# Kernel optimization log

Measured on AMD Instinct MI355X. Metric: run time of the kernel, lower is better.

## Reference

```python
import jax, jax.numpy as jnp
import numpy as np

ITERS = 10   # self.iters
REG = 0.1    # self.reg
EPS = 1e-12  # F.normalize eps


def setup_inputs() -> dict:
    key = jax.random.key(0)
    k1, k2 = jax.random.split(key)
    b, n_s, h = 64, 512, 1024
    x = jax.random.normal(k1, (b, n_s, h), dtype=jnp.float32)
    y = jax.random.normal(k2, (b, n_s, h), dtype=jnp.float32)
    return {"x": x, "y": y}


def _l2_normalize(t):
    n = jnp.sqrt(jnp.sum(t * t, axis=-1, keepdims=True))
    return t / jnp.maximum(n, EPS)


def reference(x, y):
    # CosineScorer.score(x, y, get_diag=False) with temperature=1
    xn = _l2_normalize(x)
    yn = _l2_normalize(y)
    scores = jnp.einsum('bmh,bnh->bmn', xn, yn)  # (b, n_s, n_s)
    b, m, n = scores.shape

    # uniform log marginals: -log(n_s)
    log_mu = jnp.full((b, m), -jnp.log(jnp.float32(m)), dtype=scores.dtype)
    log_nu = jnp.full((b, n), -jnp.log(jnp.float32(n)), dtype=scores.dtype)

    # log_ipot: iterative proximal point OT in log space
    A = scores / jnp.float32(REG)

    def step(carry, _):
        v, T = carry
        Q = A + T                                              # (b, m, n)
        u = log_mu - jax.nn.logsumexp(Q + v[:, None, :], axis=2)
        v_new = log_nu - jax.nn.logsumexp(Q + u[:, :, None], axis=1)
        T_new = Q + u[:, :, None] + v_new[:, None, :]
        return (v_new, T_new), None

    init = (log_nu, jnp.zeros_like(scores))
    (_, T), _ = jax.lax.scan(step, init, None, length=ITERS)

    matching = jnp.exp(T)
    return jnp.sum(scores * matching, axis=(1, 2))  # (b,)
```

## Files before the change

kernel.cpp:

```cpp
#include <hip/hip_runtime.h>
#include <hip/hip_fp16.h>

#define NB 64
#define NS 512
#define NH 1024
#define NITERS 10

#define LOG_INV_NS (-6.238324625039508f)

using half8 = _Float16 __attribute__((ext_vector_type(8)));
using f32x4 = float __attribute__((ext_vector_type(4)));

__global__ __launch_bounds__(512) void gemm_fused(
    const float* __restrict__ x, const float* __restrict__ y,
    _Float16* __restrict__ Sh) {
  __shared__ _Float16 As[2][256][40];
  __shared__ _Float16 Bs[2][256][40];
  __shared__ float invA[256], invB[256];

  int blk = blockIdx.x;
  int b = blk & 63;
  int tile = blk >> 6;
  int tm = (tile >> 1) * 256, tn = (tile & 1) * 256;
  int tid = threadIdx.x;
  int wid = tid >> 6, lane = tid & 63;
  int wr = (wid >> 2) * 128;
  int wc = (wid & 3) * 64;
  int fr = lane & 15, fq = lane >> 4;

  int srow = tid >> 1;
  int skh = (tid & 1) * 16;
  const float* xb = x + ((size_t)b * NS + tm + srow) * NH + skh;
  const float* yb = y + ((size_t)b * NS + tn + srow) * NH + skh;

  f32x4 acc[8][4] = {};
  float4 rx[4], ry[4];
  float sqx = 0.f, sqy = 0.f;

#define GLOAD(K0)                                                     \
  do {                                                                \
    const float4* px = (const float4*)(xb + (K0));                    \
    const float4* py = (const float4*)(yb + (K0));                    \
    rx[0] = px[0]; rx[1] = px[1]; rx[2] = px[2]; rx[3] = px[3];       \
    ry[0] = py[0]; ry[1] = py[1]; ry[2] = py[2]; ry[3] = py[3];       \
  } while (0)

#define CAST_WRITE(BUF)                                               \
  do {                                                                \
    alignas(16) _Float16 ta[16];                                      \
    alignas(16) _Float16 tb[16];                                      \
    _Pragma("unroll") for (int j = 0; j < 4; ++j) {                   \
      float4 v = rx[j];                                               \
      ta[4 * j + 0] = (_Float16)v.x; ta[4 * j + 1] = (_Float16)v.y;   \
      ta[4 * j + 2] = (_Float16)v.z; ta[4 * j + 3] = (_Float16)v.w;   \
      sqx += v.x * v.x + v.y * v.y + v.z * v.z + v.w * v.w;           \
    }                                                                 \
    _Pragma("unroll") for (int j = 0; j < 4; ++j) {                   \
      float4 v = ry[j];                                               \
      tb[4 * j + 0] = (_Float16)v.x; tb[4 * j + 1] = (_Float16)v.y;   \
      tb[4 * j + 2] = (_Float16)v.z; tb[4 * j + 3] = (_Float16)v.w;   \
      sqy += v.x * v.x + v.y * v.y + v.z * v.z + v.w * v.w;           \
    }                                                                 \
    *(half8*)&As[BUF][srow][skh + 0] = *(half8*)&ta[0];               \
    *(half8*)&As[BUF][srow][skh + 8] = *(half8*)&ta[8];               \
    *(half8*)&Bs[BUF][srow][skh + 0] = *(half8*)&tb[0];               \
    *(half8*)&Bs[BUF][srow][skh + 8] = *(half8*)&tb[8];               \
  } while (0)

  GLOAD(0);
  CAST_WRITE(0);
  GLOAD(32);
  asm volatile("s_waitcnt lgkmcnt(0)" ::: "memory");
  __builtin_amdgcn_sched_barrier(0);
  __builtin_amdgcn_s_barrier();
  __builtin_amdgcn_sched_barrier(0);

  for (int s = 0; s < 32; ++s) {
    int cur = s & 1;
    half8 bf[4];
#pragma unroll
    for (int j = 0; j < 4; ++j)
      bf[j] = *(const half8*)&Bs[cur][wc + 16 * j + fr][8 * fq];
    __builtin_amdgcn_s_setprio(1);
#pragma unroll
    for (int i = 0; i < 4; ++i) {
      half8 af = *(const half8*)&As[cur][wr + 16 * i + fr][8 * fq];
#pragma unroll
      for (int j = 0; j < 4; ++j)
        acc[i][j] = __builtin_amdgcn_mfma_f32_16x16x32_f16(af, bf[j], acc[i][j], 0, 0, 0);
    }
    __builtin_amdgcn_s_setprio(0);
    if (s < 31) {
      CAST_WRITE(cur ^ 1);
      if (s < 30) GLOAD((s + 2) * 32);
    }
    __builtin_amdgcn_s_setprio(1);
#pragma unroll
    for (int i = 4; i < 8; ++i) {
      half8 af = *(const half8*)&As[cur][wr + 16 * i + fr][8 * fq];
#pragma unroll
      for (int j = 0; j < 4; ++j)
        acc[i][j] = __builtin_amdgcn_mfma_f32_16x16x32_f16(af, bf[j], acc[i][j], 0, 0, 0);
    }
    __builtin_amdgcn_s_setprio(0);
    asm volatile("s_waitcnt lgkmcnt(0)" ::: "memory");
    __builtin_amdgcn_sched_barrier(0);
    __builtin_amdgcn_s_barrier();
    __builtin_amdgcn_sched_barrier(0);
  }
#undef GLOAD
#undef CAST_WRITE

  sqx += __shfl_xor(sqx, 1, 64);
  sqy += __shfl_xor(sqy, 1, 64);
  if ((tid & 1) == 0) {
    invA[srow] = 1.0f / fmaxf(sqrtf(sqx), 1e-12f);
    invB[srow] = 1.0f / fmaxf(sqrtf(sqy), 1e-12f);
  }
  __syncthreads();

  _Float16* Sb = Sh + (size_t)b * NS * NS;
#pragma unroll
  for (int i = 0; i < 8; ++i)
#pragma unroll
    for (int j = 0; j < 4; ++j) {
      int rr = wr + 16 * i + 4 * fq;
      int cc = wc + 16 * j + fr;
      float ib = invB[cc];
#pragma unroll
      for (int p = 0; p < 4; ++p)
        Sb[(size_t)(tm + rr + p) * NS + tn + cc] =
            (_Float16)(acc[i][j][p] * invA[rr + p] * ib);
    }
}

__global__ __launch_bounds__(256) void u_kernel(
    const _Float16* __restrict__ Sh, const float* __restrict__ W,
    float* __restrict__ U, float f, int first) {
  __shared__ float Wt[8][65];
  int blk = blockIdx.x;
  int bs = blk & 7, rest = blk >> 3;
  int rowgrp = rest & 31, bq = rest >> 5;
  int b = bq * 8 + bs;
  int t = threadIdx.x;
  if (!first) {
#pragma unroll
    for (int i = 0; i < 2; ++i) {
      int idx = t + 256 * i;
      Wt[idx & 7][idx >> 3] = W[b * NS + idx];
    }
    __syncthreads();
  }
  int w = t >> 6, l = t & 63;
  float wn[8];
#pragma unroll
  for (int e = 0; e < 8; ++e) wn[e] = first ? LOG_INV_NS : Wt[e][l];
  int m0 = rowgrp * 16 + w * 4;
  const _Float16* Sb = Sh + ((size_t)b * NS + m0) * NS + 8 * l;
  float sum[4] = {0.f, 0.f, 0.f, 0.f};
#pragma unroll
  for (int k = 0; k < 4; ++k) {
    half8 hv = *(const half8*)(Sb + (size_t)k * NS);
#pragma unroll
    for (int e = 0; e < 8; ++e) sum[k] += __expf(fmaf(f, (float)hv[e], wn[e]));
  }
#pragma unroll
  for (int o = 32; o; o >>= 1) {
#pragma unroll
    for (int k = 0; k < 4; ++k) sum[k] += __shfl_xor(sum[k], o, 64);
  }
  if (l == 0) {
#pragma unroll
    for (int k = 0; k < 4; ++k)
      U[b * NS + m0 + k] = LOG_INV_NS - __logf(sum[k]);
  }
}

__global__ __launch_bounds__(256) void v_kernel(
    const _Float16* __restrict__ Sh, const float* __restrict__ U,
    float* __restrict__ V, float* __restrict__ W,
    float f, int first, int last, float* __restrict__ outPart) {
  __shared__ float Ul[NS];
  __shared__ float partC[64][33];
  __shared__ float partD[64][33];
  __shared__ float redC[4][33];
  __shared__ float redD[4][33];
  int blk = blockIdx.x;
  int b = blk & 63;
  int ng = blk >> 6;
  int t = threadIdx.x;
  Ul[t] = U[b * NS + t];
  Ul[t + 256] = U[b * NS + t + 256];
  __syncthreads();

  int oct = t & 3;
  int mc = t >> 2;
  const _Float16* Sb = Sh + (size_t)b * NS * NS + (size_t)(mc * 8) * NS + ng * 32 + oct * 8;
  float c[8] = {}, d[8] = {};
#pragma unroll
  for (int i = 0; i < 8; ++i) {
    half8 hv = *(const half8*)(Sb + (size_t)i * NS);
    float um = Ul[mc * 8 + i];
#pragma unroll
    for (int e = 0; e < 8; ++e) {
      float sv = (float)hv[e];
      float ev = __expf(fmaf(f, sv, um));
      c[e] += ev;
      d[e] = fmaf(sv, ev, d[e]);
    }
  }
#pragma unroll
  for (int e = 0; e < 8; ++e) {
    partC[mc][oct * 8 + e] = c[e];
    partD[mc][oct * 8 + e] = d[e];
  }
  __syncthreads();
  {
    int ci = t & 31, seg = t >> 5;
    float cc = 0.f, dd = 0.f;
#pragma unroll
    for (int k = 0; k < 8; ++k) {
      cc += partC[seg * 8 + k][ci];
      dd += partD[seg * 8 + k][ci];
    }
    cc += __shfl_xor(cc, 32, 64);
    dd += __shfl_xor(dd, 32, 64);
    int w = t >> 6, l = t & 63;
    if (l < 32) { redC[w][l] = cc; redD[w][l] = dd; }
  }
  __syncthreads();
  if (t < 32) {
    float cc = redC[0][t] + redC[1][t] + redC[2][t] + redC[3][t];
    float vnew = LOG_INV_NS - __logf(cc);
    int n = b * NS + ng * 32 + t;
    float vold = first ? 0.f : V[n];
    V[n] = vnew;
    W[n] = 2.f * vnew - vold;
    if (last) {
      float dd = redD[0][t] + redD[1][t] + redD[2][t] + redD[3][t];
      float r = dd / cc;
      r += __shfl_xor(r, 16, 64);
      r += __shfl_xor(r, 8, 64);
      r += __shfl_xor(r, 4, 64);
      r += __shfl_xor(r, 2, 64);
      r += __shfl_xor(r, 1, 64);
      if (t == 0) outPart[b * 16 + ng] = r * (1.0f / (float)NS);
    }
  }
}

__global__ void combine_kernel(const float* __restrict__ outPart, float* __restrict__ out) {
  int b = threadIdx.x;
  float s = 0.f;
#pragma unroll
  for (int k = 0; k < 16; ++k) s += outPart[b * 16 + k];
  out[b] = s;
}

extern "C" void kernel_launch(void* const* d_in, const int* in_sizes, int n_in,
                              void* d_out, int out_size, void* d_ws, size_t ws_size,
                              hipStream_t stream) {
  (void)in_sizes; (void)n_in; (void)out_size; (void)ws_size;
  const float* x = (const float*)d_in[0];
  const float* y = (const float*)d_in[1];
  float* out = (float*)d_out;

  char* ws = (char*)d_ws;
  _Float16* Sh = (_Float16*)ws;
  float* fregion = (float*)(ws + (size_t)NB * NS * NS * 2);
  float* U = fregion;
  float* V = U + NB * NS;
  float* W = V + NB * NS;
  float* outPart = W + NB * NS;

  gemm_fused<<<256, 512, 0, stream>>>(x, y, Sh);

  for (int t = 1; t <= NITERS; ++t) {
    float f = 10.0f * (float)t;
    u_kernel<<<2048, 256, 0, stream>>>(Sh, W, U, f, t == 1 ? 1 : 0);
    v_kernel<<<1024, 256, 0, stream>>>(Sh, U, V, W, f, t == 1 ? 1 : 0,
                                       t == NITERS ? 1 : 0, outPart);
  }
  combine_kernel<<<1, 64, 0, stream>>>(outPart, out);
}
```

Measured before the change: 193.9 us.

## Shrink GEMM tile to 256x128 and double grid to fill all CUs

Changes the fused normalize+GEMM tile from 256x256 to 256x128 per block, doubling the grid from 256 to 512 blocks. Each wave now computes a 64x64 sub-tile with 4x4 accumulators, and launch bounds request more resident blocks. The setprio split is removed. The intent is better CU occupancy on a 256-CU part, at the cost of more redundant loads of x rows and lower arithmetic intensity per block.

```diff
diff --git a/kernel.cpp b/kernel.cpp
--- a/kernel.cpp
+++ b/kernel.cpp
@@ -11,30 +11,30 @@
 using half8 = _Float16 __attribute__((ext_vector_type(8)));
 using f32x4 = float __attribute__((ext_vector_type(4)));
 
-__global__ __launch_bounds__(512) void gemm_fused(
+__global__ __launch_bounds__(512, 4) void gemm_fused(
     const float* __restrict__ x, const float* __restrict__ y,
     _Float16* __restrict__ Sh) {
   __shared__ _Float16 As[2][256][40];
-  __shared__ _Float16 Bs[2][256][40];
-  __shared__ float invA[256], invB[256];
+  __shared__ _Float16 Bs[2][128][40];
+  __shared__ float invA[256], invB[128];
 
   int blk = blockIdx.x;
   int b = blk & 63;
   int tile = blk >> 6;
-  int tm = (tile >> 1) * 256, tn = (tile & 1) * 256;
+  int tm = (tile >> 2) * 256, tn = (tile & 3) * 128;
   int tid = threadIdx.x;
   int wid = tid >> 6, lane = tid & 63;
-  int wr = (wid >> 2) * 128;
-  int wc = (wid & 3) * 64;
+  int wr = (wid >> 1) * 64;
+  int wc = (wid & 1) * 64;
   int fr = lane & 15, fq = lane >> 4;
 
-  int srow = tid >> 1;
-  int skh = (tid & 1) * 16;
-  const float* xb = x + ((size_t)b * NS + tm + srow) * NH + skh;
-  const float* yb = y + ((size_t)b * NS + tn + srow) * NH + skh;
-
-  f32x4 acc[8][4] = {};
-  float4 rx[4], ry[4];
+  int srA = tid >> 1, skA = (tid & 1) * 16;
+  int srB = tid >> 2, skB = (tid & 3) * 8;
+  const float* xb = x + ((size_t)b * NS + tm + srA) * NH + skA;
+  const float* yb = y + ((size_t)b * NS + tn + srB) * NH + skB;
+
+  f32x4 acc[4][4] = {};
+  float4 rx[4], ry[2];
   float sqx = 0.f, sqy = 0.f;
 
 #define GLOAD(K0)                                                     \
@@ -42,29 +42,28 @@
     const float4* px = (const float4*)(xb + (K0));                    \
     const float4* py = (const float4*)(yb + (K0));                    \
     rx[0] = px[0]; rx[1] = px[1]; rx[2] = px[2]; rx[3] = px[3];       \
-    ry[0] = py[0]; ry[1] = py[1]; ry[2] = py[2]; ry[3] = py[3];       \
+    ry[0] = py[0]; ry[1] = py[1];                                     \
   } while (0)
 
 #define CAST_WRITE(BUF)                                               \
   do {                                                                \
     alignas(16) _Float16 ta[16];                                      \
-    alignas(16) _Float16 tb[16];                                      \
+    alignas(16) _Float16 tb[8];                                       \
     _Pragma("unroll") for (int j = 0; j < 4; ++j) {                   \
       float4 v = rx[j];                                               \
       ta[4 * j + 0] = (_Float16)v.x; ta[4 * j + 1] = (_Float16)v.y;   \
       ta[4 * j + 2] = (_Float16)v.z; ta[4 * j + 3] = (_Float16)v.w;   \
       sqx += v.x * v.x + v.y * v.y + v.z * v.z + v.w * v.w;           \
     }                                                                 \
-    _Pragma("unroll") for (int j = 0; j < 4; ++j) {                   \
+    _Pragma("unroll") for (int j = 0; j < 2; ++j) {                   \
       float4 v = ry[j];                                               \
       tb[4 * j + 0] = (_Float16)v.x; tb[4 * j + 1] = (_Float16)v.y;   \
       tb[4 * j + 2] = (_Float16)v.z; tb[4 * j + 3] = (_Float16)v.w;   \
       sqy += v.x * v.x + v.y * v.y + v.z * v.z + v.w * v.w;           \
     }                                                                 \
-    *(half8*)&As[BUF][srow][skh + 0] = *(half8*)&ta[0];               \
-    *(half8*)&As[BUF][srow][skh + 8] = *(half8*)&ta[8];               \
-    *(half8*)&Bs[BUF][srow][skh + 0] = *(half8*)&tb[0];               \
-    *(half8*)&Bs[BUF][srow][skh + 8] = *(half8*)&tb[8];               \
+    *(half8*)&As[BUF][srA][skA + 0] = *(half8*)&ta[0];                \
+    *(half8*)&As[BUF][srA][skA + 8] = *(half8*)&ta[8];                \
+    *(half8*)&Bs[BUF][srB][skB] = *(half8*)&tb[0];                    \
   } while (0)
 
   GLOAD(0);
@@ -77,32 +76,22 @@
 
   for (int s = 0; s < 32; ++s) {
     int cur = s & 1;
-    half8 bf[4];
+    half8 bf[4], af[4];
 #pragma unroll
     for (int j = 0; j < 4; ++j)
       bf[j] = *(const half8*)&Bs[cur][wc + 16 * j + fr][8 * fq];
-    __builtin_amdgcn_s_setprio(1);
-#pragma unroll
-    for (int i = 0; i < 4; ++i) {
-      half8 af = *(const half8*)&As[cur][wr + 16 * i + fr][8 * fq];
+#pragma unroll
+    for (int i = 0; i < 4; ++i)
+      af[i] = *(const half8*)&As[cur][wr + 16 * i + fr][8 * fq];
+#pragma unroll
+    for (int i = 0; i < 4; ++i)
 #pragma unroll
       for (int j = 0; j < 4; ++j)
-        acc[i][j] = __builtin_amdgcn_mfma_f32_16x16x32_f16(af, bf[j], acc[i][j], 0, 0, 0);
-    }
-    __builtin_amdgcn_s_setprio(0);
+        acc[i][j] = __builtin_amdgcn_mfma_f32_16x16x32_f16(af[i], bf[j], acc[i][j], 0, 0, 0);
     if (s < 31) {
       CAST_WRITE(cur ^ 1);
       if (s < 30) GLOAD((s + 2) * 32);
     }
-    __builtin_amdgcn_s_setprio(1);
-#pragma unroll
-    for (int i = 4; i < 8; ++i) {
-      half8 af = *(const half8*)&As[cur][wr + 16 * i + fr][8 * fq];
-#pragma unroll
-      for (int j = 0; j < 4; ++j)
-        acc[i][j] = __builtin_amdgcn_mfma_f32_16x16x32_f16(af, bf[j], acc[i][j], 0, 0, 0);
-    }
-    __builtin_amdgcn_s_setprio(0);
     asm volatile("s_waitcnt lgkmcnt(0)" ::: "memory");
     __builtin_amdgcn_sched_barrier(0);
     __builtin_amdgcn_s_barrier();
@@ -112,16 +101,15 @@
 #undef CAST_WRITE
 
   sqx += __shfl_xor(sqx, 1, 64);
+  if ((tid & 1) == 0) invA[srA] = 1.0f / fmaxf(sqrtf(sqx), 1e-12f);
   sqy += __shfl_xor(sqy, 1, 64);
-  if ((tid & 1) == 0) {
-    invA[srow] = 1.0f / fmaxf(sqrtf(sqx), 1e-12f);
-    invB[srow] = 1.0f / fmaxf(sqrtf(sqy), 1e-12f);
-  }
+  sqy += __shfl_xor(sqy, 2, 64);
+  if ((tid & 3) == 0) invB[srB] = 1.0f / fmaxf(sqrtf(sqy), 1e-12f);
   __syncthreads();
 
   _Float16* Sb = Sh + (size_t)b * NS * NS;
 #pragma unroll
-  for (int i = 0; i < 8; ++i)
+  for (int i = 0; i < 4; ++i)
 #pragma unroll
     for (int j = 0; j < 4; ++j) {
       int rr = wr + 16 * i + 4 * fq;
@@ -273,7 +261,7 @@
   float* W = V + NB * NS;
   float* outPart = W + NB * NS;
 
-  gemm_fused<<<256, 512, 0, stream>>>(x, y, Sh);
+  gemm_fused<<<512, 512, 0, stream>>>(x, y, Sh);
 
   for (int t = 1; t <= NITERS; ++t) {
     float f = 10.0f * (float)t;
```

New measurement: 224.3 us. +15.7%, slower.
